# Kernel optimization log

Measured on AMD Instinct MI355X. Metric: run time of the kernel, lower is better.

Reference implementation:

```python
import jax, jax.numpy as jnp
import numpy as np

EPS = 1e-8

def _dwconv1d(x, w, b):
    # x: [B, C, T], w: [C, 1, K] depthwise, b: [C]; 'same' padding
    y = jax.lax.conv_general_dilated(
        x, w, window_strides=(1,), padding='SAME',
        dimension_numbers=('NCH', 'OIH', 'NCH'),
        feature_group_count=x.shape[1])
    return y + b[None, :, None]

def _conv1d(x, w, b):
    # x: [B, 1, T], w: [1, 1, K], b: [1]
    y = jax.lax.conv_general_dilated(
        x, w, window_strides=(1,), padding='SAME',
        dimension_numbers=('NCH', 'OIH', 'NCH'))
    return y + b[None, :, None]

def setup_inputs() -> dict:
    key = jax.random.key(0)
    ks = jax.random.split(key, 8)
    B, F, T = 4, 256, 60000
    N_bands, N_diff, N_la, N_g, sigma_g = 8, 5, 11, 15, 3.0
    x = jax.random.uniform(ks[0], (B, F, T), dtype=jnp.float32)
    log_gamma = jnp.full((N_bands,), jnp.log(10.0), dtype=jnp.float32)
    # diff kernel: [-1, +1] centered, depthwise conv2d weight [8,1,1,5]
    dk = np.zeros((N_bands, 1, 1, N_diff), dtype=np.float32)
    dk[..., N_diff // 2] = -1.0
    dk[..., N_diff // 2 + 1] = 1.0
    diff_w = jnp.asarray(dk)
    diff_b = 0.01 * jax.random.normal(ks[1], (N_bands,), dtype=jnp.float32)
    la_w = jnp.ones((N_bands, 1, N_la), dtype=jnp.float32) / N_la
    la_b = 0.01 * jax.random.normal(ks[2], (N_bands,), dtype=jnp.float32)
    mix_w = jnp.ones((1, N_bands), dtype=jnp.float32) / N_bands
    gwin = jnp.exp(-(jnp.arange(N_g, dtype=jnp.float32) - N_g // 2) ** 2 / (2.0 * sigma_g))
    g_w = gwin.reshape(1, 1, -1)
    g_b = 0.01 * jax.random.normal(ks[3], (1,), dtype=jnp.float32)
    fc_w = jnp.ones((1, 4), dtype=jnp.float32) / 4.0
    fc_b = 0.01 * jax.random.normal(ks[4], (1,), dtype=jnp.float32)
    fg_w = gwin.reshape(1, 1, -1)
    fg_b = 0.01 * jax.random.normal(ks[5], (1,), dtype=jnp.float32)
    return dict(x=x, log_gamma=log_gamma, diff_w=diff_w, diff_b=diff_b,
                la_w=la_w, la_b=la_b, mix_w=mix_w, g_w=g_w, g_b=g_b,
                fc_w=fc_w, fc_b=fc_b, fg_w=fg_w, fg_b=fg_b)

def reference(x, log_gamma, diff_w, diff_b, la_w, la_b, mix_w, g_w, g_b,
              fc_w, fc_b, fg_w, fg_b):
    B, F, T = x.shape
    NB = log_gamma.shape[0]  # 8 bands
    Fb = F // NB
    # chunk(dim=1)+stack(dim=3)+permute(0,3,1,2) == reshape to [B, NB, Fb, T]
    xr = x.reshape(B, NB, Fb, T)
    # logarithmic compression, gamma per band
    xl = jnp.log1p(jnp.exp(log_gamma)[None, :, None, None] * xr)
    # depthwise temporal differentiation, kernel (1, N_diff), 'same'
    xd = jax.lax.conv_general_dilated(
        xl, diff_w, window_strides=(1, 1), padding='SAME',
        dimension_numbers=('NCHW', 'OIHW', 'NCHW'),
        feature_group_count=NB) + diff_b[None, :, None, None]
    # half-wave rectification (LeakyReLU, slope 0.0)
    xh = jax.nn.leaky_relu(xd, negative_slope=0.0)
    # pool over frequency -> [B, NB, T]
    xp = xh.sum(axis=2)
    # subtract local average (depthwise conv1d, ones/11)
    xs = xp - _dwconv1d(xp, la_w, la_b)
    # weighted sum over bands (Linear, no bias) -> [B, 1, T]
    xm = jnp.einsum('bct,oc->bot', xs, mix_w)
    # gaussian smoothing -> [B, T]
    xg = _conv1d(xm, g_w, g_b)[:, 0, :]
    xg = jax.nn.leaky_relu(xg, negative_slope=0.0)
    spectral_flux = xg / (xg.max(axis=1, keepdims=True) + EPS)
    # Fuser: concat 4 copies of spectral_flux along last axis -> [B, T, 4]
    conc = jnp.stack([spectral_flux] * 4, axis=-1)
    fm = jnp.einsum('btc,oc->bto', conc, fc_w) + fc_b  # [B, T, 1]
    fs = _conv1d(fm.transpose(0, 2, 1), fg_w, fg_b)    # [B, 1, T]
    fa = jax.nn.sigmoid(fs[:, 0, :])
    fused_nov = fa / (fa.max(axis=1, keepdims=True) + EPS)
    return spectral_flux, fused_nov
```

## Files before the change

kernel.cpp:

```cpp
#include <hip/hip_runtime.h>
#include <cmath>

#define T_LEN 60000
#define BATCH 4
#define NBANDS 8
#define FB 32
#define EPS 1e-8f

__global__ void k0_init(int* __restrict__ m) {
    if (threadIdx.x < 8) m[threadIdx.x] = 0;
}

__global__ __launch_bounds__(256) void k1_xp(
        const float* __restrict__ x, const float* __restrict__ log_gamma,
        const float* __restrict__ diff_w, const float* __restrict__ diff_b,
        float* __restrict__ xp) {
    __shared__ float sh[260];
    const int tid = threadIdx.x;
    const int t0 = blockIdx.x * 256;
    const int band = blockIdx.y;
    const int b = blockIdx.z;
    const float gamma = __expf(log_gamma[band]);
    float dw[5];
#pragma unroll
    for (int k = 0; k < 5; ++k) dw[k] = diff_w[band * 5 + k];
    const float db = diff_b[band];
    const size_t row0 = ((size_t)(b * 256 + band * 32)) * T_LEN;
    float acc = 0.f;
    for (int f = 0; f < 32; ++f) {
        const float* row = x + row0 + (size_t)f * T_LEN;
        __syncthreads();
        for (int i = tid; i < 260; i += 256) {
            int tt = t0 + i - 2;
            float v = 0.f;
            if (tt >= 0 && tt < T_LEN) v = __logf(fmaf(gamma, row[tt], 1.0f));
            sh[i] = v;
        }
        __syncthreads();
        float xd = db;
#pragma unroll
        for (int k = 0; k < 5; ++k) xd = fmaf(dw[k], sh[tid + k], xd);
        acc += fmaxf(xd, 0.f);
    }
    const int t = t0 + tid;
    if (t < T_LEN) xp[((size_t)(b * NBANDS + band)) * T_LEN + t] = acc;
}

__global__ __launch_bounds__(256) void k2_xg(
        const float* __restrict__ xp,
        const float* __restrict__ la_w, const float* __restrict__ la_b,
        const float* __restrict__ mix_w, const float* __restrict__ g_w,
        const float* __restrict__ g_b,
        float* __restrict__ xg, int* __restrict__ m1_bits) {
    __shared__ float shxp[NBANDS][280];
    __shared__ float shxm[272];
    __shared__ float red[4];
    const int tid = threadIdx.x;
    const int t0 = blockIdx.x * 256;
    const int b = blockIdx.y;
    for (int c = 0; c < NBANDS; ++c) {
        const float* row = xp + ((size_t)(b * NBANDS + c)) * T_LEN;
        for (int i = tid; i < 280; i += 256) {
            int tt = t0 + i - 12;
            shxp[c][i] = (tt >= 0 && tt < T_LEN) ? row[tt] : 0.f;
        }
    }
    __syncthreads();
    for (int j = tid; j < 270; j += 256) {
        int tp = t0 - 7 + j;
        float xm = 0.f;
        if (tp >= 0 && tp < T_LEN) {
            for (int c = 0; c < NBANDS; ++c) {
                float conv = la_b[c];
#pragma unroll
                for (int k = 0; k < 11; ++k)
                    conv = fmaf(la_w[c * 11 + k], shxp[c][j + k], conv);
                xm = fmaf(mix_w[c], shxp[c][j + 5] - conv, xm);
            }
        }
        shxm[j] = xm;
    }
    __syncthreads();
    const int t = t0 + tid;
    float v = g_b[0];
#pragma unroll
    for (int k = 0; k < 15; ++k) v = fmaf(g_w[k], shxm[tid + k], v);
    v = fmaxf(v, 0.f);
    if (t < T_LEN) xg[(size_t)b * T_LEN + t] = v;
    else v = 0.f;
#pragma unroll
    for (int off = 32; off > 0; off >>= 1) v = fmaxf(v, __shfl_down(v, off));
    if ((tid & 63) == 0) red[tid >> 6] = v;
    __syncthreads();
    if (tid == 0) {
        float m = fmaxf(fmaxf(red[0], red[1]), fmaxf(red[2], red[3]));
        atomicMax(&m1_bits[b], __float_as_int(m));
    }
}

__global__ __launch_bounds__(256) void k3a(
        const float* __restrict__ xg, const int* __restrict__ m1_bits,
        const float* __restrict__ fc_w, const float* __restrict__ fc_b,
        const float* __restrict__ fg_w, const float* __restrict__ fg_b,
        float* __restrict__ sf_out, float* __restrict__ fa_out,
        int* __restrict__ m2_bits) {
    __shared__ float shfm[272];
    __shared__ float red[4];
    const int tid = threadIdx.x;
    const int t0 = blockIdx.x * 256;
    const int b = blockIdx.y;
    const float inv = 1.f / (__int_as_float(m1_bits[b]) + EPS);
    const float sfc = fc_w[0] + fc_w[1] + fc_w[2] + fc_w[3];
    const float fcb = fc_b[0];
    for (int i = tid; i < 270; i += 256) {
        int tt = t0 + i - 7;
        float v = 0.f;
        if (tt >= 0 && tt < T_LEN)
            v = fmaf(sfc, xg[(size_t)b * T_LEN + tt] * inv, fcb);
        shfm[i] = v;
    }
    __syncthreads();
    const int t = t0 + tid;
    float fs = fg_b[0];
#pragma unroll
    for (int k = 0; k < 15; ++k) fs = fmaf(fg_w[k], shfm[tid + k], fs);
    float sig = 1.f / (1.f + __expf(-fs));
    float v;
    if (t < T_LEN) {
        sf_out[(size_t)b * T_LEN + t] = xg[(size_t)b * T_LEN + t] * inv;
        fa_out[(size_t)b * T_LEN + t] = sig;
        v = sig;
    } else {
        v = 0.f;
    }
#pragma unroll
    for (int off = 32; off > 0; off >>= 1) v = fmaxf(v, __shfl_down(v, off));
    if ((tid & 63) == 0) red[tid >> 6] = v;
    __syncthreads();
    if (tid == 0) {
        float m = fmaxf(fmaxf(red[0], red[1]), fmaxf(red[2], red[3]));
        atomicMax(&m2_bits[b], __float_as_int(m));
    }
}

__global__ void k3b(float* __restrict__ fa, const int* __restrict__ m2_bits) {
    int idx = blockIdx.x * 256 + threadIdx.x;
    if (idx >= BATCH * T_LEN) return;
    int b = idx / T_LEN;
    float inv = 1.f / (__int_as_float(m2_bits[b]) + EPS);
    fa[idx] = fa[idx] * inv;
}

extern "C" void kernel_launch(void* const* d_in, const int* in_sizes, int n_in,
                              void* d_out, int out_size, void* d_ws, size_t ws_size,
                              hipStream_t stream) {
    const float* x    = (const float*)d_in[0];
    const float* lg   = (const float*)d_in[1];
    const float* dw   = (const float*)d_in[2];
    const float* db   = (const float*)d_in[3];
    const float* law  = (const float*)d_in[4];
    const float* lab  = (const float*)d_in[5];
    const float* mixw = (const float*)d_in[6];
    const float* gw   = (const float*)d_in[7];
    const float* gb   = (const float*)d_in[8];
    const float* fcw  = (const float*)d_in[9];
    const float* fcb  = (const float*)d_in[10];
    const float* fgw  = (const float*)d_in[11];
    const float* fgb  = (const float*)d_in[12];

    float* ws = (float*)d_ws;
    float* xp = ws;
    float* xg = ws + (size_t)BATCH * NBANDS * T_LEN;
    int*   m1 = (int*)(xg + (size_t)BATCH * T_LEN);
    int*   m2 = m1 + 4;

    float* sf_out = (float*)d_out;
    float* fn_out = sf_out + (size_t)BATCH * T_LEN;

    const int tb = (T_LEN + 255) / 256;

    k0_init<<<dim3(1), dim3(64), 0, stream>>>(m1);
    k1_xp<<<dim3(tb, NBANDS, BATCH), dim3(256), 0, stream>>>(x, lg, dw, db, xp);
    k2_xg<<<dim3(tb, BATCH), dim3(256), 0, stream>>>(xp, law, lab, mixw, gw, gb, xg, m1);
    k3a<<<dim3(tb, BATCH), dim3(256), 0, stream>>>(xg, m1, fcw, fcb, fgw, fgb,
                                                   sf_out, fn_out, m2);
    k3b<<<dim3((BATCH * T_LEN + 255) / 256), dim3(256), 0, stream>>>(fn_out, m2);
}
```

Measured before the change: 476.4 us.

## Register-blocked k1 with shuffles, fused 25-tap k2 filter, drop init kernel

k1 now has each thread process 8 consecutive time steps with float4 loads. It takes the stencil halo from neighbour lanes through wave shuffles instead of staging every frequency row in shared memory behind two barriers per row. k2 folds the local-average subtraction, band mix and Gaussian smoothing into one precomputed 25-tap filter per band, computes 4 outputs per thread over 1024-sample tiles, and handles the sequence edges with a direct slow path. The zero-initialisation of the max slots moves into k1 so k0 is no longer launched. The risks are a reordered floating-point sum and a possible race: the slots are zeroed inside a block of k1, which still finishes before k2 runs on the same stream.

```diff
diff --git a/kernel.cpp b/kernel.cpp
--- a/kernel.cpp
+++ b/kernel.cpp
@@ -7,90 +7,178 @@
 #define FB 32
 #define EPS 1e-8f
 
-__global__ void k0_init(int* __restrict__ m) {
-    if (threadIdx.x < 8) m[threadIdx.x] = 0;
+__device__ __forceinline__ float logload(const float* row, int t, float gamma) {
+    return (t >= 0 && t < T_LEN) ? __logf(fmaf(gamma, row[t], 1.0f)) : 0.f;
 }
 
 __global__ __launch_bounds__(256) void k1_xp(
         const float* __restrict__ x, const float* __restrict__ log_gamma,
         const float* __restrict__ diff_w, const float* __restrict__ diff_b,
-        float* __restrict__ xp) {
-    __shared__ float sh[260];
-    const int tid = threadIdx.x;
-    const int t0 = blockIdx.x * 256;
-    const int band = blockIdx.y;
-    const int b = blockIdx.z;
+        float* __restrict__ xp, int* __restrict__ mslots) {
+    if (blockIdx.x == 0 && blockIdx.y == 0 && blockIdx.z == 0 && threadIdx.x < 8)
+        mslots[threadIdx.x] = 0;
+    const int tid = threadIdx.x, lane = tid & 63;
+    const int band = blockIdx.y, b = blockIdx.z;
+    const int t0 = blockIdx.x * 2048 + tid * 8;
     const float gamma = __expf(log_gamma[band]);
     float dw[5];
 #pragma unroll
     for (int k = 0; k < 5; ++k) dw[k] = diff_w[band * 5 + k];
     const float db = diff_b[band];
-    const size_t row0 = ((size_t)(b * 256 + band * 32)) * T_LEN;
-    float acc = 0.f;
-    for (int f = 0; f < 32; ++f) {
-        const float* row = x + row0 + (size_t)f * T_LEN;
-        __syncthreads();
-        for (int i = tid; i < 260; i += 256) {
-            int tt = t0 + i - 2;
-            float v = 0.f;
-            if (tt >= 0 && tt < T_LEN) v = __logf(fmaf(gamma, row[tt], 1.0f));
-            sh[i] = v;
-        }
-        __syncthreads();
-        float xd = db;
-#pragma unroll
-        for (int k = 0; k < 5; ++k) xd = fmaf(dw[k], sh[tid + k], xd);
-        acc += fmaxf(xd, 0.f);
-    }
-    const int t = t0 + tid;
-    if (t < T_LEN) xp[((size_t)(b * NBANDS + band)) * T_LEN + t] = acc;
-}
-
+    const float* base = x + ((size_t)(b * NBANDS + band) * FB) * T_LEN;
+    float acc[8];
+#pragma unroll
+    for (int j = 0; j < 8; ++j) acc[j] = 0.f;
+#pragma unroll 2
+    for (int f = 0; f < FB; ++f) {
+        const float* row = base + (size_t)f * T_LEN;
+        float lv[8];
+        if (t0 + 7 < T_LEN) {
+            float4 v0 = *(const float4*)(row + t0);
+            float4 v1 = *(const float4*)(row + t0 + 4);
+            lv[0] = __logf(fmaf(gamma, v0.x, 1.f));
+            lv[1] = __logf(fmaf(gamma, v0.y, 1.f));
+            lv[2] = __logf(fmaf(gamma, v0.z, 1.f));
+            lv[3] = __logf(fmaf(gamma, v0.w, 1.f));
+            lv[4] = __logf(fmaf(gamma, v1.x, 1.f));
+            lv[5] = __logf(fmaf(gamma, v1.y, 1.f));
+            lv[6] = __logf(fmaf(gamma, v1.z, 1.f));
+            lv[7] = __logf(fmaf(gamma, v1.w, 1.f));
+        } else {
+#pragma unroll
+            for (int j = 0; j < 8; ++j) {
+                int t = t0 + j;
+                lv[j] = (t < T_LEN) ? __logf(fmaf(gamma, row[t], 1.f)) : 0.f;
+            }
+        }
+        float l2 = __shfl_up(lv[6], 1);
+        float l1 = __shfl_up(lv[7], 1);
+        float r0 = __shfl_down(lv[0], 1);
+        float r1 = __shfl_down(lv[1], 1);
+        if (lane == 0)       { l2 = logload(row, t0 - 2, gamma); l1 = logload(row, t0 - 1, gamma); }
+        else if (lane == 63) { r0 = logload(row, t0 + 8, gamma); r1 = logload(row, t0 + 9, gamma); }
+        float e[12] = {l2, l1, lv[0], lv[1], lv[2], lv[3], lv[4], lv[5], lv[6], lv[7], r0, r1};
+#pragma unroll
+        for (int j = 0; j < 8; ++j) {
+            float xd = db;
+#pragma unroll
+            for (int k = 0; k < 5; ++k) xd = fmaf(dw[k], e[j + k], xd);
+            acc[j] += fmaxf(xd, 0.f);
+        }
+    }
+    if (t0 < T_LEN) {
+        float* op = xp + ((size_t)(b * NBANDS + band)) * T_LEN + t0;
+        if (t0 + 7 < T_LEN) {
+            *(float4*)op       = make_float4(acc[0], acc[1], acc[2], acc[3]);
+            *(float4*)(op + 4) = make_float4(acc[4], acc[5], acc[6], acc[7]);
+        } else {
+#pragma unroll
+            for (int j = 0; j < 8; ++j)
+                if (t0 + j < T_LEN) op[j] = acc[j];
+        }
+    }
+}
+
+#define K2_TILE 1024
+#define SW 1056
 __global__ __launch_bounds__(256) void k2_xg(
         const float* __restrict__ xp,
         const float* __restrict__ la_w, const float* __restrict__ la_b,
         const float* __restrict__ mix_w, const float* __restrict__ g_w,
         const float* __restrict__ g_b,
         float* __restrict__ xg, int* __restrict__ m1_bits) {
-    __shared__ float shxp[NBANDS][280];
-    __shared__ float shxm[272];
+    __shared__ float sh[NBANDS][SW];
+    __shared__ float H[NBANDS][28];
     __shared__ float red[4];
     const int tid = threadIdx.x;
-    const int t0 = blockIdx.x * 256;
+    const int T0 = blockIdx.x * K2_TILE;
     const int b = blockIdx.y;
+    const float* xpb = xp + (size_t)b * NBANDS * T_LEN;
+    for (int idx = tid; idx < NBANDS * (SW / 4); idx += 256) {
+        int c = idx / (SW / 4);
+        int i4 = idx % (SW / 4);
+        int g = T0 - 16 + 4 * i4;
+        const float* rowp = xpb + (size_t)c * T_LEN;
+        float4 v;
+        if (g >= 0 && g + 3 < T_LEN) {
+            v = *(const float4*)(rowp + g);
+        } else {
+            v.x = (g + 0 >= 0 && g + 0 < T_LEN) ? rowp[g + 0] : 0.f;
+            v.y = (g + 1 >= 0 && g + 1 < T_LEN) ? rowp[g + 1] : 0.f;
+            v.z = (g + 2 >= 0 && g + 2 < T_LEN) ? rowp[g + 2] : 0.f;
+            v.w = (g + 3 >= 0 && g + 3 < T_LEN) ? rowp[g + 3] : 0.f;
+        }
+        *(float4*)&sh[c][4 * i4] = v;
+    }
+    if (tid < 200) {
+        int c = tid / 25, m = tid % 25;
+        int klo = m - 14 > 0 ? m - 14 : 0;
+        int khi = m < 10 ? m : 10;
+        float mw = mix_w[c], s = 0.f;
+        for (int k = klo; k <= khi; ++k)
+            s += g_w[m - k] * (mw * ((k == 5 ? 1.f : 0.f) - la_w[c * 11 + k]));
+        H[c][m] = s;
+    }
+    float Sg = 0.f;
+#pragma unroll
+    for (int j = 0; j < 15; ++j) Sg += g_w[j];
+    float C0 = 0.f;
+#pragma unroll
+    for (int c = 0; c < NBANDS; ++c) C0 -= mix_w[c] * la_b[c];
+    const float cst = g_b[0] + Sg * C0;
+    __syncthreads();
+    const int basei = 4 * tid + 4;
+    float a0 = cst, a1 = cst, a2 = cst, a3 = cst;
+#pragma unroll 1
     for (int c = 0; c < NBANDS; ++c) {
-        const float* row = xp + ((size_t)(b * NBANDS + c)) * T_LEN;
-        for (int i = tid; i < 280; i += 256) {
-            int tt = t0 + i - 12;
-            shxp[c][i] = (tt >= 0 && tt < T_LEN) ? row[tt] : 0.f;
-        }
-    }
-    __syncthreads();
-    for (int j = tid; j < 270; j += 256) {
-        int tp = t0 - 7 + j;
-        float xm = 0.f;
-        if (tp >= 0 && tp < T_LEN) {
-            for (int c = 0; c < NBANDS; ++c) {
-                float conv = la_b[c];
-#pragma unroll
-                for (int k = 0; k < 11; ++k)
-                    conv = fmaf(la_w[c * 11 + k], shxp[c][j + k], conv);
-                xm = fmaf(mix_w[c], shxp[c][j + 5] - conv, xm);
+        float w[28];
+#pragma unroll
+        for (int q = 0; q < 7; ++q) {
+            float4 v = *(const float4*)&sh[c][basei + 4 * q];
+            w[4 * q] = v.x; w[4 * q + 1] = v.y; w[4 * q + 2] = v.z; w[4 * q + 3] = v.w;
+        }
+#pragma unroll
+        for (int m = 0; m < 25; ++m) {
+            float Hc = H[c][m];
+            a0 = fmaf(Hc, w[m], a0);
+            a1 = fmaf(Hc, w[m + 1], a1);
+            a2 = fmaf(Hc, w[m + 2], a2);
+            a3 = fmaf(Hc, w[m + 3], a3);
+        }
+    }
+    float vout[4] = {a0, a1, a2, a3};
+    float vmax = 0.f;
+#pragma unroll
+    for (int j = 0; j < 4; ++j) {
+        int t = T0 + 4 * tid + j;
+        float v = vout[j];
+        if (t < 7 || (t >= T_LEN - 7 && t < T_LEN)) {
+            v = g_b[0];
+            for (int jj = 0; jj < 15; ++jj) {
+                int tp = t + jj - 7;
+                if (tp < 0 || tp >= T_LEN) continue;
+                float xm = C0;
+                for (int c = 0; c < NBANDS; ++c) {
+                    float mw = mix_w[c];
+                    const float* rowp = xpb + (size_t)c * T_LEN;
+                    for (int k = 0; k < 11; ++k) {
+                        int ti = tp + k - 5;
+                        float xv = (ti >= 0 && ti < T_LEN) ? rowp[ti] : 0.f;
+                        xm = fmaf(mw * ((k == 5 ? 1.f : 0.f) - la_w[c * 11 + k]), xv, xm);
+                    }
+                }
+                v = fmaf(g_w[jj], xm, v);
             }
         }
-        shxm[j] = xm;
-    }
-    __syncthreads();
-    const int t = t0 + tid;
-    float v = g_b[0];
-#pragma unroll
-    for (int k = 0; k < 15; ++k) v = fmaf(g_w[k], shxm[tid + k], v);
-    v = fmaxf(v, 0.f);
-    if (t < T_LEN) xg[(size_t)b * T_LEN + t] = v;
-    else v = 0.f;
-#pragma unroll
-    for (int off = 32; off > 0; off >>= 1) v = fmaxf(v, __shfl_down(v, off));
-    if ((tid & 63) == 0) red[tid >> 6] = v;
+        if (t < T_LEN) {
+            v = fmaxf(v, 0.f);
+            xg[(size_t)b * T_LEN + t] = v;
+            vmax = fmaxf(vmax, v);
+        }
+    }
+#pragma unroll
+    for (int off = 32; off > 0; off >>= 1) vmax = fmaxf(vmax, __shfl_down(vmax, off));
+    if ((tid & 63) == 0) red[tid >> 6] = vmax;
     __syncthreads();
     if (tid == 0) {
         float m = fmaxf(fmaxf(red[0], red[1]), fmaxf(red[2], red[3]));
@@ -172,17 +260,17 @@
     float* xp = ws;
     float* xg = ws + (size_t)BATCH * NBANDS * T_LEN;
     int*   m1 = (int*)(xg + (size_t)BATCH * T_LEN);
-    int*   m2 = m1 + 4;
 
     float* sf_out = (float*)d_out;
     float* fn_out = sf_out + (size_t)BATCH * T_LEN;
 
-    const int tb = (T_LEN + 255) / 256;
-
-    k0_init<<<dim3(1), dim3(64), 0, stream>>>(m1);
-    k1_xp<<<dim3(tb, NBANDS, BATCH), dim3(256), 0, stream>>>(x, lg, dw, db, xp);
-    k2_xg<<<dim3(tb, BATCH), dim3(256), 0, stream>>>(xp, law, lab, mixw, gw, gb, xg, m1);
-    k3a<<<dim3(tb, BATCH), dim3(256), 0, stream>>>(xg, m1, fcw, fcb, fgw, fgb,
-                                                   sf_out, fn_out, m2);
-    k3b<<<dim3((BATCH * T_LEN + 255) / 256), dim3(256), 0, stream>>>(fn_out, m2);
-}
+    const int tb256 = (T_LEN + 255) / 256;
+
+    k1_xp<<<dim3((T_LEN + 2047) / 2048, NBANDS, BATCH), dim3(256), 0, stream>>>(
+        x, lg, dw, db, xp, m1);
+    k2_xg<<<dim3((T_LEN + K2_TILE - 1) / K2_TILE, BATCH), dim3(256), 0, stream>>>(
+        xp, law, lab, mixw, gw, gb, xg, m1);
+    k3a<<<dim3(tb256, BATCH), dim3(256), 0, stream>>>(
+        xg, m1, fcw, fcb, fgw, fgb, sf_out, fn_out, m1 + 4);
+    k3b<<<dim3((BATCH * T_LEN + 255) / 256), dim3(256), 0, stream>>>(fn_out, m1 + 4);
+}
```

Result: slower. 561.9 us (+17.9%).
